# Kernel tuning notes

Measured on AMD Instinct MI355X. Metric: run time of the kernel, lower is better.

Reference implementation:

```python
import jax, jax.numpy as jnp
import numpy as np

# Static conv hyperparameters (match init_kwargs)
STRIDE = (1, 1)
PAD = (1, 1)
DIL = (1, 1)
GROUPS = 1
DG = 1  # num_deformable_groups


def setup_inputs() -> dict:
    key = jax.random.key(0)
    k1, k2, k3 = jax.random.split(key, 3)
    B, C, H, W = 4, 256, 64, 64
    OC, kh, kw = 256, 3, 3
    x = jax.random.normal(k1, (B, C, H, W), dtype=jnp.float32)
    # offset: [B, DG*2*kh*kw, Ho, Wo], ordered (tap, [dy, dx]) per deformable group
    offset = jax.random.normal(k2, (B, DG * 2 * kh * kw, H, W), dtype=jnp.float32)
    n = C * kh * kw
    stdv = 1.0 / np.sqrt(n)
    weight = jax.random.uniform(k3, (OC, C // GROUPS, kh, kw), dtype=jnp.float32,
                                minval=-stdv, maxval=stdv)
    return {"x": x, "offset": offset, "weight": weight}


def _deform_conv(x, offset, weight):
    B, C, H, W = x.shape
    OC, Cg_w, kh, kw = weight.shape
    sh, sw = STRIDE
    ph, pw = PAD
    dh, dw = DIL
    Ho = (H + 2 * ph - (dh * (kh - 1) + 1)) // sh + 1
    Wo = (W + 2 * pw - (dw * (kw - 1) + 1)) // sw + 1
    K = kh * kw
    Cg = C // DG  # channels per deformable group

    # offsets: [B, DG, K, 2, Ho, Wo]; channel 0 = dy (h), channel 1 = dx (w)
    off = offset.reshape(B, DG, K, 2, Ho, Wo)

    # base (undeformed) sampling positions per tap
    ki, kj = jnp.meshgrid(jnp.arange(kh), jnp.arange(kw), indexing='ij')
    base_h = (jnp.arange(Ho) * sh - ph)[None, :] + (ki.reshape(-1) * dh)[:, None]  # [K, Ho]
    base_w = (jnp.arange(Wo) * sw - pw)[None, :] + (kj.reshape(-1) * dw)[:, None]  # [K, Wo]

    pos_h = base_h[None, None, :, :, None].astype(x.dtype) + off[:, :, :, 0]  # [B,DG,K,Ho,Wo]
    pos_w = base_w[None, None, :, None, :].astype(x.dtype) + off[:, :, :, 1]  # [B,DG,K,Ho,Wo]

    h0f = jnp.floor(pos_h)
    w0f = jnp.floor(pos_w)
    lh = pos_h - h0f  # fractional parts
    lw = pos_w - w0f
    h0 = h0f.astype(jnp.int32)
    w0 = w0f.astype(jnp.int32)

    xg = x.reshape(B, DG, Cg, H * W)

    def gather(hi, wi):
        # zero-padded gather: out-of-range corners contribute 0 (mmcv DCNv1 semantics)
        valid = (hi >= 0) & (hi < H) & (wi >= 0) & (wi < W)  # [B,DG,K,Ho,Wo]
        idx = jnp.clip(hi, 0, H - 1) * W + jnp.clip(wi, 0, W - 1)
        flat = idx.reshape(B, DG, 1, K * Ho * Wo)
        vals = jnp.take_along_axis(
            xg, jnp.broadcast_to(flat, (B, DG, Cg, K * Ho * Wo)), axis=3)
        vals = vals.reshape(B, DG, Cg, K, Ho, Wo)
        return vals * valid[:, :, None].astype(x.dtype)

    # bilinear interpolation over 4 corners -> im2col columns [B,DG,Cg,K,Ho,Wo]
    cols = (gather(h0, w0) * ((1 - lh) * (1 - lw))[:, :, None]
            + gather(h0, w0 + 1) * ((1 - lh) * lw)[:, :, None]
            + gather(h0 + 1, w0) * (lh * (1 - lw))[:, :, None]
            + gather(h0 + 1, w0 + 1) * (lh * lw)[:, :, None])

    # grouped GEMM: columns x weight
    cols = cols.reshape(B, GROUPS, C // GROUPS, K, Ho, Wo)
    wg = weight.reshape(GROUPS, OC // GROUPS, Cg_w, K)
    out = jnp.einsum('gock,bgckhw->bgohw', wg, cols)
    return out.reshape(B, OC, Ho, Wo)


def reference(x, offset, weight):
    return _deform_conv(x, offset, weight)
```

## Files before the change

### kernel.cpp

```cpp
#include <hip/hip_runtime.h>
#include <hip/hip_bf16.h>
#include <math.h>


constexpr int B  = 4;
constexpr int C  = 256;
constexpr int H  = 64;
constexpr int W  = 64;
constexpr int OC = 256;
constexpr int Ho = 64;
constexpr int Wo = 64;

constexpr int NT     = 64;
constexpr int CHUNKS = 72;
constexpr int WROW   = 40;

constexpr size_t WB_ELTS  = (size_t)CHUNKS * 16 * 512;
constexpr size_t XB_ELTS  = (size_t)B * 8 * 4096 * 32;
constexpr size_t OUT_ELTS = (size_t)B * OC * Ho * Wo;

typedef __attribute__((ext_vector_type(8))) short bf16x8;
typedef __attribute__((ext_vector_type(4))) float f32x4;

__device__ __forceinline__ float bf_lo(unsigned u) {
    union { unsigned i; float f; } c; c.i = u << 16; return c.f;
}
__device__ __forceinline__ float bf_hi(unsigned u) {
    union { unsigned i; float f; } c; c.i = u & 0xffff0000u; return c.f;
}
__device__ __forceinline__ ushort fbf(float f) {
    __hip_bfloat16 h = __float2bfloat16(f); return *(ushort*)&h;
}

__global__ __launch_bounds__(256)
void prep_all(const float* __restrict__ x, const float* __restrict__ wt,
              ushort* __restrict__ xb, ushort* __restrict__ wB)
{
    __shared__ ushort sx[128 * WROW];
    __shared__ ushort sw[CHUNKS * WROW];
    const int t = threadIdx.x;

    if (blockIdx.x < 1024) {
        const int blk = blockIdx.x;
        const int hwb = blk & 31;
        const int cb  = (blk >> 5) & 7;
        const int b   = blk >> 8;
        const int hw0 = hwb << 7;
        const int lhw = t & 127, chalf = t >> 7;
        #pragma unroll
        for (int i = 0; i < 16; ++i) {
            const int c = i * 2 + chalf;
            sx[lhw * WROW + c] =
                fbf(x[(((size_t)(b * 256 + cb * 32 + c)) << 12) + hw0 + lhw]);
        }
        __syncthreads();
        const int whw = t >> 1, wh = t & 1;
        const uint4 v0 = *(const uint4*)&sx[whw * WROW + wh * 16];
        const uint4 v1 = *(const uint4*)&sx[whw * WROW + wh * 16 + 8];
        uint4* dst = (uint4*)(xb + ((size_t)((b * 8 + cb) * 4096 + hw0) << 5));
        dst[whw * 4 + wh * 2 + 0] = v0;
        dst[whw * 4 + wh * 2 + 1] = v1;
    } else {
        const int oc = blockIdx.x - 1024;
        const int c  = t, chb = c >> 5, kk = c & 31;
        const float* wp = wt + ((size_t)oc * C + c) * 9;
        #pragma unroll
        for (int tap = 0; tap < 9; ++tap)
            sw[(tap * 8 + chb) * WROW + kk] = fbf(wp[tap]);
        __syncthreads();
        const int og = oc >> 4, mr = oc & 15;
        for (int i = t; i < CHUNKS * 4; i += 256) {
            const int ch = i >> 2, kq = i & 3;
            *(uint4*)(wB + ((size_t)ch * 16 + og) * 512 + (kq * 16 + mr) * 8) =
                *(const uint4*)&sw[ch * WROW + kq * 8];
        }
    }
}

struct GathRegs { uint4 c00, c01, c10, c11; float4 mw; };

__global__ __launch_bounds__(512, 4)
void dcn_mfma(const ushort* __restrict__ xb, const float* __restrict__ off,
              const ushort* __restrict__ wB, float* __restrict__ po)
{
    __shared__ __align__(16) ushort s_col[2][2][NT * WROW];
    __shared__ __align__(16) float4 s_mw[9 * NT];
    __shared__ __align__(8)  int2   s_midx[9 * NT];

    const int xcd = blockIdx.x & 7;
    const int ii  = blockIdx.x >> 3;
    const int b   = xcd & 3;
    const int khalf = ii & 1;
    const int ho  = ((xcd >> 2) << 5) + (ii >> 1);
    const int ch0 = khalf * 36;
    float* outp = po + (size_t)khalf * OUT_ELTS;
    const int tid = threadIdx.x;

    for (int s = tid; s < 9 * NT; s += 512) {
        const int n   = s & 63;
        const int tap = s >> 6;
        const float dy = off[((size_t)(b * 18 + 2 * tap)     * Ho + ho) * Wo + n];
        const float dx = off[((size_t)(b * 18 + 2 * tap + 1) * Ho + ho) * Wo + n];
        const float ph = (float)(ho - 1 + tap / 3) + dy;
        const float pw = (float)(n  - 1 + tap % 3) + dx;
        const float h0f = floorf(ph), w0f = floorf(pw);
        const int h0 = (int)h0f, w0 = (int)w0f;
        const float lh = ph - h0f, lw = pw - w0f;
        const int wb = min(max(w0, 0), W - 2);
        const int ht = min(max(h0, 0), H - 1);
        const int hb = min(max(h0 + 1, 0), H - 1);
        const float s0 = (wb == w0) ? (1.f - lw) : ((wb == w0 + 1) ? lw : 0.f);
        const float s1 = (wb + 1 == w0 + 1) ? lw : ((wb + 1 == w0) ? (1.f - lw) : 0.f);
        const float wtp = (h0 >= 0 && h0 < H)         ? (1.f - lh) : 0.f;
        const float wbt = (h0 + 1 >= 0 && h0 + 1 < H) ? lh         : 0.f;
        s_midx[s] = make_int2(ht * W + wb, hb * W + wb);
        s_mw[s]   = make_float4(wtp * s0, wtp * s1, wbt * s0, wbt * s1);
    }

    const int lane = tid & 63;
    const int wv   = tid >> 6;
    const int kq   = lane >> 4;
    const int mr   = lane & 15;

    const int kc_t = tid >> 8;
    const int st   = tid & 255;
    const int sn   = st >> 2;
    const int sgg  = st & 3;
    const ushort* xb_sg = xb + ((size_t)b << 20) + (sgg << 3);

    f32x4 acc[2][4];
    #pragma unroll
    for (int mt = 0; mt < 2; ++mt)
        #pragma unroll
        for (int nt = 0; nt < 4; ++nt)
            acc[mt][nt] = (f32x4){0.f, 0.f, 0.f, 0.f};

    auto issueg = [&](int p, GathRegs& g) {
        const int ch  = ch0 + 2 * p + kc_t;
        const int tap = ch >> 3;
        const int cb  = ch & 7;
        const int2 mi = s_midx[tap * NT + sn];
        g.mw = s_mw[tap * NT + sn];
        const ushort* xp = xb_sg + ((size_t)cb << 17);
        g.c00 = *(const uint4*)(xp + ((size_t)mi.x << 5));
        g.c01 = *(const uint4*)(xp + (((size_t)mi.x + 1) << 5));
        g.c10 = *(const uint4*)(xp + ((size_t)mi.y << 5));
        g.c11 = *(const uint4*)(xp + (((size_t)mi.y + 1) << 5));
    };
    auto sampfma = [&](const GathRegs& g, int buf) {
        union { ushort pk[8]; uint4 v; } u;
        const unsigned a00[4] = {g.c00.x, g.c00.y, g.c00.z, g.c00.w};
        const unsigned a01[4] = {g.c01.x, g.c01.y, g.c01.z, g.c01.w};
        const unsigned a10[4] = {g.c10.x, g.c10.y, g.c10.z, g.c10.w};
        const unsigned a11[4] = {g.c11.x, g.c11.y, g.c11.z, g.c11.w};
        #pragma unroll
        for (int j = 0; j < 4; ++j) {
            const float vlo = g.mw.x * bf_lo(a00[j]) + g.mw.y * bf_lo(a01[j])
                            + g.mw.z * bf_lo(a10[j]) + g.mw.w * bf_lo(a11[j]);
            const float vhi = g.mw.x * bf_hi(a00[j]) + g.mw.y * bf_hi(a01[j])
                            + g.mw.z * bf_hi(a10[j]) + g.mw.w * bf_hi(a11[j]);
            u.pk[2 * j]     = fbf(vlo);
            u.pk[2 * j + 1] = fbf(vhi);
        }
        *(uint4*)&s_col[buf][kc_t][sn * WROW + sgg * 8] = u.v;
    };
    auto phase = [&](int p, const GathRegs& gcur, int buf) {
        sampfma(gcur, buf);
        bf16x8 wf[2][2];
        const int chb = ch0 + 2 * p;
        #pragma unroll
        for (int kc = 0; kc < 2; ++kc)
            #pragma unroll
            for (int mt = 0; mt < 2; ++mt)
                wf[kc][mt] = *(const bf16x8*)
                    (wB + ((size_t)(chb + kc) * 16 + wv * 2 + mt) * 512 + lane * 8);
        asm volatile("s_waitcnt lgkmcnt(0)" ::: "memory");
        __builtin_amdgcn_s_barrier();
        __builtin_amdgcn_sched_barrier(0);
        __builtin_amdgcn_s_setprio(1);
        #pragma unroll
        for (int kc = 0; kc < 2; ++kc)
            #pragma unroll
            for (int nt = 0; nt < 4; ++nt) {
                const bf16x8 bfr = *(const bf16x8*)
                    &s_col[buf][kc][(nt * 16 + mr) * WROW + kq * 8];
                #pragma unroll
                for (int mt = 0; mt < 2; ++mt)
                    acc[mt][nt] = __builtin_amdgcn_mfma_f32_16x16x32_bf16(
                        wf[kc][mt], bfr, acc[mt][nt], 0, 0, 0);
            }
        __builtin_amdgcn_s_setprio(0);
    };

    __syncthreads();

    GathRegs gA, gB;
    issueg(0, gA);

    #pragma unroll 1
    for (int it = 0; it < 9; ++it) {
        issueg(2 * it + 1, gB);
        phase(2 * it, gA, 0);
        if (it < 8) issueg(2 * it + 2, gA);
        phase(2 * it + 1, gB, 1);
    }

    #pragma unroll
    for (int mt = 0; mt < 2; ++mt)
        #pragma unroll
        for (int nt = 0; nt < 4; ++nt)
            #pragma unroll
            for (int r = 0; r < 4; ++r) {
                const int oc = wv * 32 + mt * 16 + kq * 4 + r;
                const int wo = nt * 16 + mr;
                outp[((size_t)(b * OC + oc) * Ho + ho) * Wo + wo] = acc[mt][nt][r];
            }
}

__global__ __launch_bounds__(256)
void reduce2(const float4* __restrict__ p0, const float4* __restrict__ p1,
             float4* __restrict__ out)
{
    const int i = blockIdx.x * 256 + threadIdx.x;
    const float4 a = p0[i], b = p1[i];
    out[i] = make_float4(a.x + b.x, a.y + b.y, a.z + b.z, a.w + b.w);
}

extern "C" void kernel_launch(void* const* d_in, const int* in_sizes, int n_in,
                              void* d_out, int out_size, void* d_ws, size_t ws_size,
                              hipStream_t stream)
{
    const float* x   = (const float*)d_in[0];
    const float* off = (const float*)d_in[1];
    const float* wt  = (const float*)d_in[2];
    float* out = (float*)d_out;

    ushort* wB = (ushort*)d_ws;
    ushort* xb = wB + WB_ELTS;
    float*  po = (float*)(xb + XB_ELTS);

    prep_all<<<1280, 256, 0, stream>>>(x, wt, xb, wB);
    dcn_mfma<<<512, 512, 0, stream>>>(xb, off, wB, po);
    reduce2<<<(int)(OUT_ELTS / 4 / 256), 256, 0, stream>>>(
        (const float4*)po, (const float4*)(po + OUT_ELTS), (float4*)out);
}
```

Before: 113.6 us.

## Split K four ways and fuse reduction via last-arriver atomic ticket

The main kernel now splits the channel/tap reduction into four slices of 18 chunks instead of two of 36, doubling the grid to 1024 blocks for more parallelism. The separate reduce kernel is removed. Each block writes its partial, increments a per-row atomic counter, and the last-arriving block sums the other three partials into the output. This costs four partial buffers of traffic and an atomic handshake per row, in exchange for higher occupancy and one fewer launch.

After: 425.1 us. +274.2%, slower.

```diff
diff --git a/kernel.cpp b/kernel.cpp
--- a/kernel.cpp
+++ b/kernel.cpp
@@ -13,6 +13,7 @@
 
 constexpr int NT     = 64;
 constexpr int CHUNKS = 72;
+constexpr int KCH    = 18;
 constexpr int WROW   = 40;
 
 constexpr size_t WB_ELTS  = (size_t)CHUNKS * 16 * 512;
@@ -34,7 +35,8 @@
 
 __global__ __launch_bounds__(256)
 void prep_all(const float* __restrict__ x, const float* __restrict__ wt,
-              ushort* __restrict__ xb, ushort* __restrict__ wB)
+              ushort* __restrict__ xb, ushort* __restrict__ wB,
+              int* __restrict__ flags)
 {
     __shared__ ushort sx[128 * WROW];
     __shared__ ushort sw[CHUNKS * WROW];
@@ -62,6 +64,7 @@
         dst[whw * 4 + wh * 2 + 1] = v1;
     } else {
         const int oc = blockIdx.x - 1024;
+        if (oc == 0 && t < 256) flags[t] = 0;
         const int c  = t, chb = c >> 5, kk = c & 31;
         const float* wp = wt + ((size_t)oc * C + c) * 9;
         #pragma unroll
@@ -81,20 +84,23 @@
 
 __global__ __launch_bounds__(512, 4)
 void dcn_mfma(const ushort* __restrict__ xb, const float* __restrict__ off,
-              const ushort* __restrict__ wB, float* __restrict__ po)
+              const ushort* __restrict__ wB, float* __restrict__ po,
+              float* __restrict__ out, int* __restrict__ flags)
 {
     __shared__ __align__(16) ushort s_col[2][2][NT * WROW];
     __shared__ __align__(16) float4 s_mw[9 * NT];
     __shared__ __align__(8)  int2   s_midx[9 * NT];
-
-    const int xcd = blockIdx.x & 7;
-    const int ii  = blockIdx.x >> 3;
-    const int b   = xcd & 3;
-    const int khalf = ii & 1;
-    const int ho  = ((xcd >> 2) << 5) + (ii >> 1);
-    const int ch0 = khalf * 36;
-    float* outp = po + (size_t)khalf * OUT_ELTS;
-    const int tid = threadIdx.x;
+    __shared__ int s_ticket;
+
+    const int xcd   = blockIdx.x & 7;
+    const int inner = blockIdx.x >> 3;
+    const int kidx  = inner & 3;
+    const int rowloc= inner >> 2;
+    const int b     = xcd & 3;
+    const int ho    = ((xcd >> 2) << 5) + rowloc;
+    const int row   = (b << 6) + ho;
+    const int ch0   = kidx * KCH;
+    const int tid   = threadIdx.x;
 
     for (int s = tid; s < 9 * NT; s += 512) {
         const int n   = s & 63;
@@ -198,13 +204,15 @@
     issueg(0, gA);
 
     #pragma unroll 1
-    for (int it = 0; it < 9; ++it) {
+    for (int it = 0; it < 4; ++it) {
         issueg(2 * it + 1, gB);
         phase(2 * it, gA, 0);
-        if (it < 8) issueg(2 * it + 2, gA);
+        issueg(2 * it + 2, gA);
         phase(2 * it + 1, gB, 1);
     }
-
+    phase(8, gA, 0);
+
+    float* pop = po + (size_t)kidx * OUT_ELTS;
     #pragma unroll
     for (int mt = 0; mt < 2; ++mt)
         #pragma unroll
@@ -213,17 +221,33 @@
             for (int r = 0; r < 4; ++r) {
                 const int oc = wv * 32 + mt * 16 + kq * 4 + r;
                 const int wo = nt * 16 + mr;
-                outp[((size_t)(b * OC + oc) * Ho + ho) * Wo + wo] = acc[mt][nt][r];
+                pop[((size_t)(b * OC + oc) * Ho + ho) * Wo + wo] = acc[mt][nt][r];
             }
-}
-
-__global__ __launch_bounds__(256)
-void reduce2(const float4* __restrict__ p0, const float4* __restrict__ p1,
-             float4* __restrict__ out)
-{
-    const int i = blockIdx.x * 256 + threadIdx.x;
-    const float4 a = p0[i], b = p1[i];
-    out[i] = make_float4(a.x + b.x, a.y + b.y, a.z + b.z, a.w + b.w);
+
+    __threadfence();
+    __syncthreads();
+    if (tid == 0)
+        s_ticket = __hip_atomic_fetch_add(&flags[row], 1,
+                                          __ATOMIC_ACQ_REL,
+                                          __HIP_MEMORY_SCOPE_AGENT);
+    __syncthreads();
+    if (s_ticket == 3) {
+        const float* q0 = po + (size_t)((kidx + 1) & 3) * OUT_ELTS;
+        const float* q1 = po + (size_t)((kidx + 2) & 3) * OUT_ELTS;
+        const float* q2 = po + (size_t)((kidx + 3) & 3) * OUT_ELTS;
+        #pragma unroll
+        for (int mt = 0; mt < 2; ++mt)
+            #pragma unroll
+            for (int nt = 0; nt < 4; ++nt)
+                #pragma unroll
+                for (int r = 0; r < 4; ++r) {
+                    const int oc = wv * 32 + mt * 16 + kq * 4 + r;
+                    const int wo = nt * 16 + mr;
+                    const size_t base =
+                        ((size_t)(b * OC + oc) * Ho + ho) * Wo + wo;
+                    out[base] = acc[mt][nt][r] + q0[base] + q1[base] + q2[base];
+                }
+    }
 }
 
 extern "C" void kernel_launch(void* const* d_in, const int* in_sizes, int n_in,
@@ -235,12 +259,11 @@
     const float* wt  = (const float*)d_in[2];
     float* out = (float*)d_out;
 
-    ushort* wB = (ushort*)d_ws;
+    int*    flags = (int*)d_ws;
+    ushort* wB = (ushort*)d_ws + 512;
     ushort* xb = wB + WB_ELTS;
     float*  po = (float*)(xb + XB_ELTS);
 
-    prep_all<<<1280, 256, 0, stream>>>(x, wt, xb, wB);
-    dcn_mfma<<<512, 512, 0, stream>>>(xb, off, wB, po);
-    reduce2<<<(int)(OUT_ELTS / 4 / 256), 256, 0, stream>>>(
-        (const float4*)po, (const float4*)(po + OUT_ELTS), (float4*)out);
-}
+    prep_all<<<1280, 256, 0, stream>>>(x, wt, xb, wB, flags);
+    dcn_mfma<<<1024, 512, 0, stream>>>(xb, off, wB, po, out, flags);
+}
```

## Split reduction dimension four ways and reduce four partial outputs

Applied to the files above, without the earlier changes.

The GEMM's reduction dimension is split into four quarters of 18 chunks instead of two halves of 36, doubling the grid to 1024 blocks. Each block runs a shorter pipelined loop and writes its own partial output buffer, and a four-way reduce kernel sums them. The aim is more parallelism and better occupancy on the GPU, at the cost of twice the partial-output traffic, more workspace, and repeating the per-block offset and bilinear-weight setup in twice as many blocks.

New measurement: 119.6 us. +5.3%, slower.

```diff
diff --git a/kernel.cpp b/kernel.cpp
--- a/kernel.cpp
+++ b/kernel.cpp
@@ -13,6 +13,7 @@
 
 constexpr int NT     = 64;
 constexpr int CHUNKS = 72;
+constexpr int KCH    = 18;
 constexpr int WROW   = 40;
 
 constexpr size_t WB_ELTS  = (size_t)CHUNKS * 16 * 512;
@@ -87,14 +88,14 @@
     __shared__ __align__(16) float4 s_mw[9 * NT];
     __shared__ __align__(8)  int2   s_midx[9 * NT];
 
-    const int xcd = blockIdx.x & 7;
-    const int ii  = blockIdx.x >> 3;
-    const int b   = xcd & 3;
-    const int khalf = ii & 1;
-    const int ho  = ((xcd >> 2) << 5) + (ii >> 1);
-    const int ch0 = khalf * 36;
-    float* outp = po + (size_t)khalf * OUT_ELTS;
-    const int tid = threadIdx.x;
+    const int xcd   = blockIdx.x & 7;
+    const int inner = blockIdx.x >> 3;
+    const int kidx  = inner & 3;
+    const int rowloc= inner >> 2;
+    const int b     = xcd & 3;
+    const int ho    = ((xcd >> 2) << 5) + rowloc;
+    const int ch0   = kidx * KCH;
+    const int tid   = threadIdx.x;
 
     for (int s = tid; s < 9 * NT; s += 512) {
         const int n   = s & 63;
@@ -198,13 +199,15 @@
     issueg(0, gA);
 
     #pragma unroll 1
-    for (int it = 0; it < 9; ++it) {
+    for (int it = 0; it < 4; ++it) {
         issueg(2 * it + 1, gB);
         phase(2 * it, gA, 0);
-        if (it < 8) issueg(2 * it + 2, gA);
+        issueg(2 * it + 2, gA);
         phase(2 * it + 1, gB, 1);
     }
-
+    phase(8, gA, 0);
+
+    float* pop = po + (size_t)kidx * OUT_ELTS;
     #pragma unroll
     for (int mt = 0; mt < 2; ++mt)
         #pragma unroll
@@ -213,17 +216,19 @@
             for (int r = 0; r < 4; ++r) {
                 const int oc = wv * 32 + mt * 16 + kq * 4 + r;
                 const int wo = nt * 16 + mr;
-                outp[((size_t)(b * OC + oc) * Ho + ho) * Wo + wo] = acc[mt][nt][r];
+                pop[((size_t)(b * OC + oc) * Ho + ho) * Wo + wo] = acc[mt][nt][r];
             }
 }
 
 __global__ __launch_bounds__(256)
-void reduce2(const float4* __restrict__ p0, const float4* __restrict__ p1,
+void reduce4(const float4* __restrict__ p0, const float4* __restrict__ p1,
+             const float4* __restrict__ p2, const float4* __restrict__ p3,
              float4* __restrict__ out)
 {
     const int i = blockIdx.x * 256 + threadIdx.x;
-    const float4 a = p0[i], b = p1[i];
-    out[i] = make_float4(a.x + b.x, a.y + b.y, a.z + b.z, a.w + b.w);
+    const float4 a = p0[i], b = p1[i], c = p2[i], d = p3[i];
+    out[i] = make_float4(a.x + b.x + c.x + d.x, a.y + b.y + c.y + d.y,
+                         a.z + b.z + c.z + d.z, a.w + b.w + c.w + d.w);
 }
 
 extern "C" void kernel_launch(void* const* d_in, const int* in_sizes, int n_in,
@@ -240,7 +245,9 @@
     float*  po = (float*)(xb + XB_ELTS);
 
     prep_all<<<1280, 256, 0, stream>>>(x, wt, xb, wB);
-    dcn_mfma<<<512, 512, 0, stream>>>(xb, off, wB, po);
-    reduce2<<<(int)(OUT_ELTS / 4 / 256), 256, 0, stream>>>(
-        (const float4*)po, (const float4*)(po + OUT_ELTS), (float4*)out);
-}
+    dcn_mfma<<<1024, 512, 0, stream>>>(xb, off, wB, po);
+    reduce4<<<(int)(OUT_ELTS / 4 / 256), 256, 0, stream>>>(
+        (const float4*)po, (const float4*)(po + OUT_ELTS),
+        (const float4*)(po + 2 * OUT_ELTS), (const float4*)(po + 3 * OUT_ELTS),
+        (float4*)out);
+}
```

## Compute sampling metadata per thread in registers and issue weight loads before sampling

Applied to the files above, without the earlier changes.

Drops the shared-memory table of bilinear indices and weights that was built in a prologue. Each thread now computes its own metadata in registers, lazily, whenever its tap changes. This removes the prologue, its barrier and the LDS reads. The weight-fragment global loads are also moved ahead of the bilinear sampling so their latency overlaps the interpolation arithmetic. The cost is that offset loads and metadata math now sit inside the main loop, with some redundant recomputation across threads, and register pressure may rise.

New measurement: 123.0 us. +8.2%, slower.

```diff
diff --git a/kernel.cpp b/kernel.cpp
--- a/kernel.cpp
+++ b/kernel.cpp
@@ -13,6 +13,7 @@
 
 constexpr int NT     = 64;
 constexpr int CHUNKS = 72;
+constexpr int KCH    = 36;
 constexpr int WROW   = 40;
 
 constexpr size_t WB_ELTS  = (size_t)CHUNKS * 16 * 512;
@@ -84,38 +85,15 @@
               const ushort* __restrict__ wB, float* __restrict__ po)
 {
     __shared__ __align__(16) ushort s_col[2][2][NT * WROW];
-    __shared__ __align__(16) float4 s_mw[9 * NT];
-    __shared__ __align__(8)  int2   s_midx[9 * NT];
 
     const int xcd = blockIdx.x & 7;
     const int ii  = blockIdx.x >> 3;
     const int b   = xcd & 3;
     const int khalf = ii & 1;
     const int ho  = ((xcd >> 2) << 5) + (ii >> 1);
-    const int ch0 = khalf * 36;
+    const int ch0 = khalf * KCH;
     float* outp = po + (size_t)khalf * OUT_ELTS;
     const int tid = threadIdx.x;
-
-    for (int s = tid; s < 9 * NT; s += 512) {
-        const int n   = s & 63;
-        const int tap = s >> 6;
-        const float dy = off[((size_t)(b * 18 + 2 * tap)     * Ho + ho) * Wo + n];
-        const float dx = off[((size_t)(b * 18 + 2 * tap + 1) * Ho + ho) * Wo + n];
-        const float ph = (float)(ho - 1 + tap / 3) + dy;
-        const float pw = (float)(n  - 1 + tap % 3) + dx;
-        const float h0f = floorf(ph), w0f = floorf(pw);
-        const int h0 = (int)h0f, w0 = (int)w0f;
-        const float lh = ph - h0f, lw = pw - w0f;
-        const int wb = min(max(w0, 0), W - 2);
-        const int ht = min(max(h0, 0), H - 1);
-        const int hb = min(max(h0 + 1, 0), H - 1);
-        const float s0 = (wb == w0) ? (1.f - lw) : ((wb == w0 + 1) ? lw : 0.f);
-        const float s1 = (wb + 1 == w0 + 1) ? lw : ((wb + 1 == w0) ? (1.f - lw) : 0.f);
-        const float wtp = (h0 >= 0 && h0 < H)         ? (1.f - lh) : 0.f;
-        const float wbt = (h0 + 1 >= 0 && h0 + 1 < H) ? lh         : 0.f;
-        s_midx[s] = make_int2(ht * W + wb, hb * W + wb);
-        s_mw[s]   = make_float4(wtp * s0, wtp * s1, wbt * s0, wbt * s1);
-    }
 
     const int lane = tid & 63;
     const int wv   = tid >> 6;
@@ -135,12 +113,37 @@
         for (int nt = 0; nt < 4; ++nt)
             acc[mt][nt] = (f32x4){0.f, 0.f, 0.f, 0.f};
 
+    int   ctap = -1;
+    int2  mi   = make_int2(0, 0);
+    float4 mwv = make_float4(0.f, 0.f, 0.f, 0.f);
+    auto upd_meta = [&](int p) {
+        const int ch  = ch0 + 2 * p + kc_t;
+        const int tap = ch >> 3;
+        if (tap != ctap) {
+            ctap = tap;
+            const float dy = off[((size_t)(b * 18 + 2 * tap)     * Ho + ho) * Wo + sn];
+            const float dx = off[((size_t)(b * 18 + 2 * tap + 1) * Ho + ho) * Wo + sn];
+            const float ph = (float)(ho - 1 + tap / 3) + dy;
+            const float pw = (float)(sn - 1 + tap % 3) + dx;
+            const float h0f = floorf(ph), w0f = floorf(pw);
+            const int h0 = (int)h0f, w0 = (int)w0f;
+            const float lh = ph - h0f, lw = pw - w0f;
+            const int wb = min(max(w0, 0), W - 2);
+            const int ht = min(max(h0, 0), H - 1);
+            const int hb = min(max(h0 + 1, 0), H - 1);
+            const float s0 = (wb == w0) ? (1.f - lw) : ((wb == w0 + 1) ? lw : 0.f);
+            const float s1 = (wb + 1 == w0 + 1) ? lw : ((wb + 1 == w0) ? (1.f - lw) : 0.f);
+            const float wtp = (h0 >= 0 && h0 < H)         ? (1.f - lh) : 0.f;
+            const float wbt = (h0 + 1 >= 0 && h0 + 1 < H) ? lh         : 0.f;
+            mi  = make_int2(ht * W + wb, hb * W + wb);
+            mwv = make_float4(wtp * s0, wtp * s1, wbt * s0, wbt * s1);
+        }
+    };
+
     auto issueg = [&](int p, GathRegs& g) {
         const int ch  = ch0 + 2 * p + kc_t;
-        const int tap = ch >> 3;
         const int cb  = ch & 7;
-        const int2 mi = s_midx[tap * NT + sn];
-        g.mw = s_mw[tap * NT + sn];
+        g.mw = mwv;
         const ushort* xp = xb_sg + ((size_t)cb << 17);
         g.c00 = *(const uint4*)(xp + ((size_t)mi.x << 5));
         g.c01 = *(const uint4*)(xp + (((size_t)mi.x + 1) << 5));
@@ -165,7 +168,6 @@
         *(uint4*)&s_col[buf][kc_t][sn * WROW + sgg * 8] = u.v;
     };
     auto phase = [&](int p, const GathRegs& gcur, int buf) {
-        sampfma(gcur, buf);
         bf16x8 wf[2][2];
         const int chb = ch0 + 2 * p;
         #pragma unroll
@@ -174,6 +176,7 @@
             for (int mt = 0; mt < 2; ++mt)
                 wf[kc][mt] = *(const bf16x8*)
                     (wB + ((size_t)(chb + kc) * 16 + wv * 2 + mt) * 512 + lane * 8);
+        sampfma(gcur, buf);
         asm volatile("s_waitcnt lgkmcnt(0)" ::: "memory");
         __builtin_amdgcn_s_barrier();
         __builtin_amdgcn_sched_barrier(0);
@@ -192,16 +195,19 @@
         __builtin_amdgcn_s_setprio(0);
     };
 
-    __syncthreads();
-
     GathRegs gA, gB;
+    upd_meta(0);
     issueg(0, gA);
 
     #pragma unroll 1
     for (int it = 0; it < 9; ++it) {
+        upd_meta(2 * it + 1);
         issueg(2 * it + 1, gB);
         phase(2 * it, gA, 0);
-        if (it < 8) issueg(2 * it + 2, gA);
+        if (it < 8) {
+            upd_meta(2 * it + 2);
+            issueg(2 * it + 2, gA);
+        }
         phase(2 * it + 1, gB, 1);
     }
 
```
